# Kernel optimization log

Hardware: AMD Instinct MI355X
Metric: run time of the kernel (lower is better)

Reference implementation:

```python
import jax, jax.numpy as jnp
import numpy as np

D_MODEL = 1024
N_HEADS = 16
D_K = D_MODEL // N_HEADS
D_FF = 4096
EPS = 1e-5


def layer_norm(x, g, b):
    mu = jnp.mean(x, axis=-1, keepdims=True)
    var = jnp.var(x, axis=-1, keepdims=True)
    return (x - mu) * jax.lax.rsqrt(var + EPS) * g + b


def setup_inputs() -> dict:
    key = jax.random.key(0)
    ks = jax.random.split(key, 16)
    B, S = 4, 2048
    s_in = 1.0 / np.sqrt(D_MODEL)
    s_ff = 1.0 / np.sqrt(D_FF)
    return {
        "x": jax.random.normal(ks[0], (B, S, D_MODEL), jnp.float32),
        "mask": jnp.ones((B, 1, 1, S), jnp.int32),
        "Wq": jax.random.normal(ks[1], (D_MODEL, D_MODEL), jnp.float32) * s_in,
        "bq": jnp.zeros((D_MODEL,), jnp.float32),
        "Wk": jax.random.normal(ks[2], (D_MODEL, D_MODEL), jnp.float32) * s_in,
        "bk": jnp.zeros((D_MODEL,), jnp.float32),
        "Wv": jax.random.normal(ks[3], (D_MODEL, D_MODEL), jnp.float32) * s_in,
        "bv": jnp.zeros((D_MODEL,), jnp.float32),
        "Wo": jax.random.normal(ks[4], (D_MODEL, D_MODEL), jnp.float32) * s_in,
        "bo": jnp.zeros((D_MODEL,), jnp.float32),
        "W1": jax.random.normal(ks[5], (D_MODEL, D_FF), jnp.float32) * s_in,
        "b1": jnp.zeros((D_FF,), jnp.float32),
        "W2": jax.random.normal(ks[6], (D_FF, D_MODEL), jnp.float32) * s_ff,
        "b2": jnp.zeros((D_MODEL,), jnp.float32),
        "ln1_g": jnp.ones((D_MODEL,), jnp.float32),
        "ln1_b": jnp.zeros((D_MODEL,), jnp.float32),
        "ln2_g": jnp.ones((D_MODEL,), jnp.float32),
        "ln2_b": jnp.zeros((D_MODEL,), jnp.float32),
    }


def reference(x, mask, Wq, bq, Wk, bk, Wv, bv, Wo, bo, W1, b1, W2, b2,
              ln1_g, ln1_b, ln2_g, ln2_b):
    B, S, _ = x.shape
    h = layer_norm(x, ln1_g, ln1_b)  # norm1(x), used for q/k/v
    # project and split heads: [B,S,D] -> [B,H,S,Dk]
    def heads(t):
        return t.reshape(B, S, N_HEADS, D_K).transpose(0, 2, 1, 3)
    Q = heads(h @ Wq + bq)
    K = heads(h @ Wk + bk)
    V = heads(h @ Wv + bv)
    scores = jnp.einsum('bhqd,bhkd->bhqk', Q, K) / jnp.sqrt(jnp.float32(D_K))
    scores = jnp.where(mask == 0, jnp.float32(-1e9), scores)
    attn = jax.nn.softmax(scores, axis=-1)
    out = jnp.einsum('bhqk,bhkd->bhqd', attn, V)
    out = out.transpose(0, 2, 1, 3).reshape(B, S, D_MODEL)
    attn_out = out @ Wo + bo
    x = x + attn_out
    # FFN with pre-norm (torch nn.GELU default = exact erf gelu)
    h2 = layer_norm(x, ln2_g, ln2_b)
    ff = jax.nn.gelu(h2 @ W1 + b1, approximate=False) @ W2 + b2
    return x + ff
```

## Files before the change

### kernel.cpp

```cpp
#include <hip/hip_runtime.h>
#include <stdint.h>
#include <string.h>


typedef unsigned int       u32;
typedef unsigned short     u16;
typedef __bf16 bf16x8 __attribute__((ext_vector_type(8)));
typedef float  floatx4 __attribute__((ext_vector_type(4)));

#define D_MODEL 1024
#define N_HEADS 16
#define D_K     64
#define D_FF    4096
#define S_LEN   2048
#define N_TOK   8192
#define LDQKV   3072

__device__ __forceinline__ u16 f2b(float f) {
    u32 u = __float_as_uint(f);
    u32 r = (u + 0x7fffu + ((u >> 16) & 1u)) >> 16;
    return (u16)r;
}

__device__ __forceinline__ float fast_gelu(float x) {
    float t = x * x;
    float y = x * 1.5957691216057308f * fmaf(t, 0.044715f, 1.0f);
    return x * __builtin_amdgcn_rcpf(1.0f + __expf(-y));
}

__device__ __forceinline__ void gl_lds16(const void* g, void* l) {
    __builtin_amdgcn_global_load_lds(
        (const __attribute__((address_space(1))) u32*)g,
        (__attribute__((address_space(3))) u32*)l, 16, 0, 0);
}

__global__ __launch_bounds__(256) void transpose_bf16_kernel(
    const float* __restrict__ src, u16* __restrict__ dst, int R, int C)
{
    __shared__ float tile[32][33];
    int cb = blockIdx.x * 32, rb = blockIdx.y * 32;
    int tx = threadIdx.x & 31, ty = threadIdx.x >> 5;
    #pragma unroll
    for (int yy = ty; yy < 32; yy += 8)
        tile[yy][tx] = src[(size_t)(rb + yy) * C + cb + tx];
    __syncthreads();
    #pragma unroll
    for (int yy = ty; yy < 32; yy += 8)
        dst[(size_t)(cb + yy) * R + rb + tx] = f2b(tile[tx][yy]);
}

__global__ __launch_bounds__(256) void vt_kernel(
    const u16* __restrict__ Qkv, u16* __restrict__ Vt)
{
    __shared__ u32 tile[64 * 65];
    int b = blockIdx.z, h = blockIdx.y, s0 = blockIdx.x * 64;
    int t = threadIdx.x;
    int r = t >> 2, cg = (t & 3) * 16;
    const u16* src = &Qkv[((size_t)(b * S_LEN + s0 + r)) * LDQKV + 2048 + h * D_K + cg];
    uint4 a0 = *(const uint4*)src;
    uint4 a1 = *(const uint4*)(src + 8);
    u16 vals[16];
    memcpy(vals, &a0, 16); memcpy(vals + 8, &a1, 16);
    #pragma unroll
    for (int j = 0; j < 16; j++) tile[r * 65 + cg + j] = vals[j];
    __syncthreads();
    int f = t & 63, w = t >> 6;
    u16 outv[16];
    #pragma unroll
    for (int j = 0; j < 16; j++) outv[j] = (u16)tile[(w * 16 + j) * 65 + f];
    uint4 o0, o1; memcpy(&o0, outv, 16); memcpy(&o1, outv + 8, 16);
    u16* dst = &Vt[((size_t)((b * N_HEADS + h) * D_K + f)) * S_LEN + s0 + w * 16];
    *(uint4*)dst = o0; *(uint4*)(dst + 8) = o1;
}

__global__ __launch_bounds__(256) void ln_kernel(
    const float* __restrict__ x, const float* __restrict__ g,
    const float* __restrict__ b, u16* __restrict__ out)
{
    int row = blockIdx.x;
    int t = threadIdx.x;
    const float4* xr = reinterpret_cast<const float4*>(x + (size_t)row * D_MODEL);
    float4 v = xr[t];
    float s  = v.x + v.y + v.z + v.w;
    float ss = v.x * v.x + v.y * v.y + v.z * v.z + v.w * v.w;
    #pragma unroll
    for (int off = 32; off >= 1; off >>= 1) {
        s  += __shfl_down(s,  off);
        ss += __shfl_down(ss, off);
    }
    __shared__ float red[8];
    int wid = t >> 6, ln = t & 63;
    if (ln == 0) { red[wid] = s; red[4 + wid] = ss; }
    __syncthreads();
    float S  = red[0] + red[1] + red[2] + red[3];
    float SS = red[4] + red[5] + red[6] + red[7];
    float mu  = S * (1.0f / D_MODEL);
    float var = SS * (1.0f / D_MODEL) - mu * mu;
    float rs  = rsqrtf(var + 1e-5f);
    const float4* g4 = reinterpret_cast<const float4*>(g);
    const float4* b4 = reinterpret_cast<const float4*>(b);
    float4 gv = g4[t], bv = b4[t];
    float y0 = (v.x - mu) * rs * gv.x + bv.x;
    float y1 = (v.y - mu) * rs * gv.y + bv.y;
    float y2 = (v.z - mu) * rs * gv.z + bv.z;
    float y3 = (v.w - mu) * rs * gv.w + bv.w;
    uint2 pk;
    pk.x = (u32)f2b(y0) | ((u32)f2b(y1) << 16);
    pk.y = (u32)f2b(y2) | ((u32)f2b(y3) << 16);
    *reinterpret_cast<uint2*>(out + (size_t)row * D_MODEL + t * 4) = pk;
}

template<int MT>
__global__ __launch_bounds__(256) void gemm_bt(
    const u16* __restrict__ A, const u16* __restrict__ Bt,
    const float* __restrict__ bias, const float* __restrict__ biasK,
    const float* __restrict__ biasV, const float* __restrict__ resid,
    float* __restrict__ outF, u16* __restrict__ outB,
    int M, int N, int K, int flags)
{
    constexpr int ATILES = MT / 32;
    __shared__ u16 As[MT * 64];
    __shared__ u16 Bs[128 * 64];

    int nbx = N >> 7, nby = M / MT;
    int bid = blockIdx.x;
    int xcd = bid & 7, p = bid >> 3;
    int bandsz = nby >> 3;
    int m0 = (xcd * bandsz + p / nbx) * MT;
    int n0 = (p % nbx) * 128;

    int t = threadIdx.x;
    int wave = t >> 6, lane = t & 63, quad = lane >> 4, lr = lane & 15;
    int wm = (wave >> 1) * (MT / 2), wn = (wave & 1) * 64;

    floatx4 acc[ATILES][4] = {};

    for (int k0 = 0; k0 < K; k0 += 64) {
        #pragma unroll
        for (int i = 0; i < MT / 32; i++) {
            int s = t + i * 256;
            int row = s >> 3, g = ((s & 7) ^ (row & 7)) * 8;
            gl_lds16(&A[(size_t)(m0 + row) * K + k0 + g], &As[s * 8]);
        }
        #pragma unroll
        for (int i = 0; i < 4; i++) {
            int s = t + i * 256;
            int row = s >> 3, g = ((s & 7) ^ (row & 7)) * 8;
            gl_lds16(&Bt[(size_t)(n0 + row) * K + k0 + g], &Bs[s * 8]);
        }
        __syncthreads();

        #pragma unroll
        for (int kk = 0; kk < 2; kk++) {
            bf16x8 af[ATILES], bfr[4];
            #pragma unroll
            for (int mt = 0; mt < ATILES; mt++) {
                int row = wm + mt * 16 + lr;
                int pg = ((kk * 4 + quad) ^ (row & 7)) * 8;
                af[mt] = *reinterpret_cast<const bf16x8*>(&As[row * 64 + pg]);
            }
            #pragma unroll
            for (int nt = 0; nt < 4; nt++) {
                int row = wn + nt * 16 + lr;
                int pg = ((kk * 4 + quad) ^ (row & 7)) * 8;
                bfr[nt] = *reinterpret_cast<const bf16x8*>(&Bs[row * 64 + pg]);
            }
            #pragma unroll
            for (int mt = 0; mt < ATILES; mt++)
                #pragma unroll
                for (int nt = 0; nt < 4; nt++)
                    acc[mt][nt] = __builtin_amdgcn_mfma_f32_16x16x32_bf16(
                        af[mt], bfr[nt], acc[mt][nt], 0, 0, 0);
        }
        __syncthreads();
    }

    bool do_gelu = (flags & 1) != 0;
    #pragma unroll
    for (int mt = 0; mt < ATILES; mt++) {
        #pragma unroll
        for (int nt = 0; nt < 4; nt++) {
            int c = n0 + wn + nt * 16 + lr;
            float bsv;
            if (biasK) {
                if (c >= 2048)      bsv = biasV[c - 2048];
                else if (c >= 1024) bsv = biasK[c - 1024];
                else                bsv = bias[c];
            } else {
                bsv = bias[c];
            }
            #pragma unroll
            for (int i = 0; i < 4; i++) {
                int r = m0 + wm + mt * 16 + quad * 4 + i;
                float v = acc[mt][nt][i] + bsv;
                if (resid) v += resid[(size_t)r * N + c];
                if (do_gelu) v = fast_gelu(v);
                if (outF) outF[(size_t)r * N + c] = v;
                if (outB) outB[(size_t)r * N + c] = f2b(v);
            }
        }
    }
}

__global__ __launch_bounds__(256, 4) void attn_mfma_kernel(
    const u16* __restrict__ Qkv, const u16* __restrict__ Vt,
    const int* __restrict__ mask, u16* __restrict__ ctx)
{
    __shared__ u16 Ks[64 * 72];
    __shared__ u16 Vs[64 * 72];
    __shared__ u16 Ps[128 * 72];
    __shared__ float Ms[64];

    int b = blockIdx.z, h = blockIdx.y;
    int q0 = blockIdx.x * 128;
    int t = threadIdx.x;
    int wave = t >> 6, lane = t & 63, quad = lane >> 4, lr = lane & 15;
    int wm = wave * 32;

    bf16x8 qf[2][2];
    #pragma unroll
    for (int mt = 0; mt < 2; mt++)
        #pragma unroll
        for (int kk = 0; kk < 2; kk++)
            qf[mt][kk] = *(const bf16x8*)&Qkv[((size_t)(b * S_LEN + q0 + wm + mt * 16 + lr)) * LDQKV
                                              + h * D_K + kk * 32 + quad * 8];

    floatx4 o[2][4] = {};
    float lsum[2][4] = {};
    const float kS = 0.125f * 1.4426950408889634f;

    for (int kt = 0; kt < S_LEN / 64; kt++) {
        __syncthreads();
        {
            int row = t >> 2, cg = (t & 3) * 16;
            const u16* kg = &Qkv[((size_t)(b * S_LEN + kt * 64 + row)) * LDQKV + 1024 + h * D_K + cg];
            *(uint4*)&Ks[row * 72 + cg]     = *(const uint4*)kg;
            *(uint4*)&Ks[row * 72 + cg + 8] = *(const uint4*)(kg + 8);
            const u16* vg = &Vt[((size_t)((b * N_HEADS + h) * D_K + row)) * S_LEN + kt * 64 + cg];
            *(uint4*)&Vs[row * 72 + cg]     = *(const uint4*)vg;
            *(uint4*)&Vs[row * 72 + cg + 8] = *(const uint4*)(vg + 8);
            if (t < 64) Ms[t] = (mask[b * S_LEN + kt * 64 + t] == 0) ? -1e30f : 0.0f;
        }
        __syncthreads();

        floatx4 s[2][4] = {};
        {
            bf16x8 bk[2][4];
            #pragma unroll
            for (int kk = 0; kk < 2; kk++)
                #pragma unroll
                for (int n = 0; n < 4; n++)
                    bk[kk][n] = *(const bf16x8*)&Ks[(n * 16 + lr) * 72 + kk * 32 + quad * 8];
            __builtin_amdgcn_s_setprio(1);
            #pragma unroll
            for (int kk = 0; kk < 2; kk++)
                #pragma unroll
                for (int mt = 0; mt < 2; mt++)
                    #pragma unroll
                    for (int n = 0; n < 4; n++)
                        s[mt][n] = __builtin_amdgcn_mfma_f32_16x16x32_bf16(
                            qf[mt][kk], bk[kk][n], s[mt][n], 0, 0, 0);
            __builtin_amdgcn_s_setprio(0);
        }

        #pragma unroll
        for (int mt = 0; mt < 2; mt++) {
            #pragma unroll
            for (int n = 0; n < 4; n++) {
                float msk = Ms[n * 16 + lr];
                float p0 = __builtin_amdgcn_exp2f(fmaf(s[mt][n][0], kS, msk));
                float p1 = __builtin_amdgcn_exp2f(fmaf(s[mt][n][1], kS, msk));
                float p2 = __builtin_amdgcn_exp2f(fmaf(s[mt][n][2], kS, msk));
                float p3 = __builtin_amdgcn_exp2f(fmaf(s[mt][n][3], kS, msk));
                lsum[mt][0] += p0; lsum[mt][1] += p1;
                lsum[mt][2] += p2; lsum[mt][3] += p3;
                u32 pkA, pkB;
                asm("v_cvt_pk_bf16_f32 %0, %1, %2" : "=v"(pkA) : "v"(p0), "v"(p1));
                asm("v_cvt_pk_bf16_f32 %0, %1, %2" : "=v"(pkB) : "v"(p2), "v"(p3));
                int base = (wm + mt * 16 + quad * 4) * 72 + n * 16 + lr;
                Ps[base]           = (u16)(pkA & 0xffffu);
                Ps[base + 72]      = (u16)(pkA >> 16);
                Ps[base + 144]     = (u16)(pkB & 0xffffu);
                Ps[base + 216]     = (u16)(pkB >> 16);
            }
        }

        bf16x8 bv[4][2];
        #pragma unroll
        for (int kk = 0; kk < 2; kk++)
            #pragma unroll
            for (int n = 0; n < 4; n++)
                bv[n][kk] = *(const bf16x8*)&Vs[(n * 16 + lr) * 72 + kk * 32 + quad * 8];

        __syncthreads();

        __builtin_amdgcn_s_setprio(1);
        #pragma unroll
        for (int kk = 0; kk < 2; kk++) {
            #pragma unroll
            for (int mt = 0; mt < 2; mt++) {
                bf16x8 ap = *(const bf16x8*)&Ps[(wm + mt * 16 + lr) * 72 + kk * 32 + quad * 8];
                #pragma unroll
                for (int n = 0; n < 4; n++)
                    o[mt][n] = __builtin_amdgcn_mfma_f32_16x16x32_bf16(
                        ap, bv[n][kk], o[mt][n], 0, 0, 0);
            }
        }
        __builtin_amdgcn_s_setprio(0);
    }

    #pragma unroll
    for (int mt = 0; mt < 2; mt++)
        #pragma unroll
        for (int i = 0; i < 4; i++) {
            float v = lsum[mt][i];
            v += __shfl_xor(v, 1);
            v += __shfl_xor(v, 2);
            v += __shfl_xor(v, 4);
            v += __shfl_xor(v, 8);
            lsum[mt][i] = 1.0f / v;
        }
    #pragma unroll
    for (int mt = 0; mt < 2; mt++)
        #pragma unroll
        for (int n = 0; n < 4; n++)
            #pragma unroll
            for (int i = 0; i < 4; i++) {
                int row = q0 + wm + mt * 16 + quad * 4 + i;
                int col = h * D_K + n * 16 + lr;
                ctx[((size_t)(b * S_LEN + row)) * D_MODEL + col] =
                    f2b(o[mt][n][i] * lsum[mt][i]);
            }
}

extern "C" void kernel_launch(void* const* d_in, const int* in_sizes, int n_in,
                              void* d_out, int out_size, void* d_ws, size_t ws_size,
                              hipStream_t stream)
{
    const float* x    = (const float*)d_in[0];
    const int*   mask = (const int*)  d_in[1];
    const float* Wq   = (const float*)d_in[2];
    const float* bq   = (const float*)d_in[3];
    const float* Wk   = (const float*)d_in[4];
    const float* bk   = (const float*)d_in[5];
    const float* Wv   = (const float*)d_in[6];
    const float* bv   = (const float*)d_in[7];
    const float* Wo   = (const float*)d_in[8];
    const float* bo   = (const float*)d_in[9];
    const float* W1   = (const float*)d_in[10];
    const float* b1   = (const float*)d_in[11];
    const float* W2   = (const float*)d_in[12];
    const float* b2   = (const float*)d_in[13];
    const float* ln1g = (const float*)d_in[14];
    const float* ln1b = (const float*)d_in[15];
    const float* ln2g = (const float*)d_in[16];
    const float* ln2b = (const float*)d_in[17];
    float* out = (float*)d_out;

    char* ws = (char*)d_ws;
    const size_t MB = 1u << 20;
    u16*   wqkvT = (u16*)(ws + 0 * MB);
    u16*   woT   = (u16*)(ws + 6 * MB);
    u16*   w1T   = (u16*)(ws + 8 * MB);
    u16*   w2T   = (u16*)(ws + 16 * MB);
    u16*   h     = (u16*)(ws + 24 * MB);
    u16*   Qkv   = (u16*)(ws + 40 * MB);
    u16*   ctx   = (u16*)(ws + 88 * MB);
    float* x1    = (float*)(ws + 104 * MB);
    u16*   Vt    = h;

    bool full = ws_size >= 216 * MB;
    u16* h2  = full ? (u16*)(ws + 136 * MB) : Qkv;
    u16* ff1 = full ? (u16*)(ws + 152 * MB) : (u16*)(ws + 56 * MB);
    int nchunk = full ? 1 : 2;
    int Mc = N_TOK / nchunk;

    dim3 blk(256);

    transpose_bf16_kernel<<<dim3(32, 32),  blk, 0, stream>>>(Wq, wqkvT,             1024, 1024);
    transpose_bf16_kernel<<<dim3(32, 32),  blk, 0, stream>>>(Wk, wqkvT + 1024*1024, 1024, 1024);
    transpose_bf16_kernel<<<dim3(32, 32),  blk, 0, stream>>>(Wv, wqkvT + 2048*1024, 1024, 1024);
    transpose_bf16_kernel<<<dim3(32, 32),  blk, 0, stream>>>(Wo, woT, 1024, 1024);
    transpose_bf16_kernel<<<dim3(128, 32), blk, 0, stream>>>(W1, w1T, 1024, 4096);
    transpose_bf16_kernel<<<dim3(32, 128), blk, 0, stream>>>(W2, w2T, 4096, 1024);

    ln_kernel<<<N_TOK, blk, 0, stream>>>(x, ln1g, ln1b, h);

    gemm_bt<128><<<dim3(24 * 64), blk, 0, stream>>>(h, wqkvT, bq, bk, bv, nullptr,
                                                    nullptr, Qkv, N_TOK, LDQKV, D_MODEL, 0);

    vt_kernel<<<dim3(32, 16, 4), blk, 0, stream>>>(Qkv, Vt);

    attn_mfma_kernel<<<dim3(16, 16, 4), blk, 0, stream>>>(Qkv, Vt, mask, ctx);

    gemm_bt<64><<<dim3(8 * 128), blk, 0, stream>>>(ctx, woT, bo, nullptr, nullptr, x,
                                                   x1, nullptr, N_TOK, D_MODEL, D_MODEL, 0);

    ln_kernel<<<N_TOK, blk, 0, stream>>>(x1, ln2g, ln2b, h2);

    for (int c = 0; c < nchunk; c++) {
        size_t ro = (size_t)c * Mc * D_MODEL;
        size_t rf = (size_t)c * Mc * D_FF;
        gemm_bt<128><<<dim3(32 * (Mc / 128)), blk, 0, stream>>>(
            h2 + ro, w1T, b1, nullptr, nullptr, nullptr,
            nullptr, ff1 + (full ? rf : 0), Mc, D_FF, D_MODEL, 1);
        gemm_bt<64><<<dim3(8 * (Mc / 64)), blk, 0, stream>>>(
            ff1 + (full ? rf : 0), w2T, b2, nullptr, nullptr, x1 + ro,
            out + ro, nullptr, Mc, D_MODEL, D_FF, 0);
    }
}
```

Before: 606.1 us.

## Fuse V transpose into QKV GEMM epilogue and transpose score MFMA layout

The QKV GEMM epilogue now writes V columns directly in transposed [b,h,d,s] layout, which removes the separate vt_kernel launch and its extra read/write pass over V. The attention kernel swaps the MFMA operand order so each lane holds four consecutive keys for one query. This lets the mask load as a float4, the row sum accumulate per lane, and P be stored to LDS as a packed 8-byte write instead of four scattered u16 stores. The softmax uses __expf with a 0.125 scale instead of exp2 with a folded constant. Vt gets its own workspace region, and the final normalisation reduces across quads and then broadcasts with shuffles.

```diff
diff --git a/kernel.cpp b/kernel.cpp
--- a/kernel.cpp
+++ b/kernel.cpp
@@ -47,30 +47,6 @@
     #pragma unroll
     for (int yy = ty; yy < 32; yy += 8)
         dst[(size_t)(cb + yy) * R + rb + tx] = f2b(tile[tx][yy]);
-}
-
-__global__ __launch_bounds__(256) void vt_kernel(
-    const u16* __restrict__ Qkv, u16* __restrict__ Vt)
-{
-    __shared__ u32 tile[64 * 65];
-    int b = blockIdx.z, h = blockIdx.y, s0 = blockIdx.x * 64;
-    int t = threadIdx.x;
-    int r = t >> 2, cg = (t & 3) * 16;
-    const u16* src = &Qkv[((size_t)(b * S_LEN + s0 + r)) * LDQKV + 2048 + h * D_K + cg];
-    uint4 a0 = *(const uint4*)src;
-    uint4 a1 = *(const uint4*)(src + 8);
-    u16 vals[16];
-    memcpy(vals, &a0, 16); memcpy(vals + 8, &a1, 16);
-    #pragma unroll
-    for (int j = 0; j < 16; j++) tile[r * 65 + cg + j] = vals[j];
-    __syncthreads();
-    int f = t & 63, w = t >> 6;
-    u16 outv[16];
-    #pragma unroll
-    for (int j = 0; j < 16; j++) outv[j] = (u16)tile[(w * 16 + j) * 65 + f];
-    uint4 o0, o1; memcpy(&o0, outv, 16); memcpy(&o1, outv + 8, 16);
-    u16* dst = &Vt[((size_t)((b * N_HEADS + h) * D_K + f)) * S_LEN + s0 + w * 16];
-    *(uint4*)dst = o0; *(uint4*)(dst + 8) = o1;
 }
 
 __global__ __launch_bounds__(256) void ln_kernel(
@@ -115,7 +91,7 @@
     const u16* __restrict__ A, const u16* __restrict__ Bt,
     const float* __restrict__ bias, const float* __restrict__ biasK,
     const float* __restrict__ biasV, const float* __restrict__ resid,
-    float* __restrict__ outF, u16* __restrict__ outB,
+    float* __restrict__ outF, u16* __restrict__ outB, u16* __restrict__ outVt,
     int M, int N, int K, int flags)
 {
     constexpr int ATILES = MT / 32;
@@ -189,6 +165,17 @@
             } else {
                 bsv = bias[c];
             }
+            if (outVt && c >= 2048) {
+                int r0 = m0 + wm + mt * 16 + quad * 4;
+                int hb = (c - 2048) >> 6, f = (c - 2048) & 63;
+                int bb = r0 >> 11, sIn = r0 & 2047;
+                u32 w0 = (u32)f2b(acc[mt][nt][0] + bsv) | ((u32)f2b(acc[mt][nt][1] + bsv) << 16);
+                u32 w1 = (u32)f2b(acc[mt][nt][2] + bsv) | ((u32)f2b(acc[mt][nt][3] + bsv) << 16);
+                uint2 pk2; pk2.x = w0; pk2.y = w1;
+                *reinterpret_cast<uint2*>(
+                    &outVt[((size_t)((bb * N_HEADS + hb) * D_K + f)) * S_LEN + sIn]) = pk2;
+                continue;
+            }
             #pragma unroll
             for (int i = 0; i < 4; i++) {
                 int r = m0 + wm + mt * 16 + quad * 4 + i;
@@ -226,8 +213,7 @@
                                               + h * D_K + kk * 32 + quad * 8];
 
     floatx4 o[2][4] = {};
-    float lsum[2][4] = {};
-    const float kS = 0.125f * 1.4426950408889634f;
+    float lsum[2] = {0.0f, 0.0f};
 
     for (int kt = 0; kt < S_LEN / 64; kt++) {
         __syncthreads();
@@ -259,7 +245,7 @@
                     #pragma unroll
                     for (int n = 0; n < 4; n++)
                         s[mt][n] = __builtin_amdgcn_mfma_f32_16x16x32_bf16(
-                            qf[mt][kk], bk[kk][n], s[mt][n], 0, 0, 0);
+                            bk[kk][n], qf[mt][kk], s[mt][n], 0, 0, 0);
             __builtin_amdgcn_s_setprio(0);
         }
 
@@ -267,21 +253,17 @@
         for (int mt = 0; mt < 2; mt++) {
             #pragma unroll
             for (int n = 0; n < 4; n++) {
-                float msk = Ms[n * 16 + lr];
-                float p0 = __builtin_amdgcn_exp2f(fmaf(s[mt][n][0], kS, msk));
-                float p1 = __builtin_amdgcn_exp2f(fmaf(s[mt][n][1], kS, msk));
-                float p2 = __builtin_amdgcn_exp2f(fmaf(s[mt][n][2], kS, msk));
-                float p3 = __builtin_amdgcn_exp2f(fmaf(s[mt][n][3], kS, msk));
-                lsum[mt][0] += p0; lsum[mt][1] += p1;
-                lsum[mt][2] += p2; lsum[mt][3] += p3;
-                u32 pkA, pkB;
-                asm("v_cvt_pk_bf16_f32 %0, %1, %2" : "=v"(pkA) : "v"(p0), "v"(p1));
-                asm("v_cvt_pk_bf16_f32 %0, %1, %2" : "=v"(pkB) : "v"(p2), "v"(p3));
-                int base = (wm + mt * 16 + quad * 4) * 72 + n * 16 + lr;
-                Ps[base]           = (u16)(pkA & 0xffffu);
-                Ps[base + 72]      = (u16)(pkA >> 16);
-                Ps[base + 144]     = (u16)(pkB & 0xffffu);
-                Ps[base + 216]     = (u16)(pkB >> 16);
+                const float4 mv = *reinterpret_cast<const float4*>(&Ms[n * 16 + quad * 4]);
+                float p0 = __expf(fmaf(s[mt][n][0], 0.125f, mv.x));
+                float p1 = __expf(fmaf(s[mt][n][1], 0.125f, mv.y));
+                float p2 = __expf(fmaf(s[mt][n][2], 0.125f, mv.z));
+                float p3 = __expf(fmaf(s[mt][n][3], 0.125f, mv.w));
+                lsum[mt] += (p0 + p1) + (p2 + p3);
+                u32 w0, w1;
+                asm("v_cvt_pk_bf16_f32 %0, %1, %2" : "=v"(w0) : "v"(p0), "v"(p1));
+                asm("v_cvt_pk_bf16_f32 %0, %1, %2" : "=v"(w1) : "v"(p2), "v"(p3));
+                uint2 pk2; pk2.x = w0; pk2.y = w1;
+                *reinterpret_cast<uint2*>(&Ps[(wm + mt * 16 + lr) * 72 + n * 16 + quad * 4]) = pk2;
             }
         }
 
@@ -309,19 +291,19 @@
         __builtin_amdgcn_s_setprio(0);
     }
 
-    #pragma unroll
-    for (int mt = 0; mt < 2; mt++)
-        #pragma unroll
-        for (int i = 0; i < 4; i++) {
-            float v = lsum[mt][i];
-            v += __shfl_xor(v, 1);
-            v += __shfl_xor(v, 2);
-            v += __shfl_xor(v, 4);
-            v += __shfl_xor(v, 8);
-            lsum[mt][i] = 1.0f / v;
-        }
-    #pragma unroll
-    for (int mt = 0; mt < 2; mt++)
+    float inv[2];
+    #pragma unroll
+    for (int mt = 0; mt < 2; mt++) {
+        float v = lsum[mt];
+        v += __shfl_xor(v, 16);
+        v += __shfl_xor(v, 32);
+        inv[mt] = 1.0f / v;
+    }
+    #pragma unroll
+    for (int mt = 0; mt < 2; mt++) {
+        float iv[4];
+        #pragma unroll
+        for (int i = 0; i < 4; i++) iv[i] = __shfl(inv[mt], quad * 4 + i);
         #pragma unroll
         for (int n = 0; n < 4; n++)
             #pragma unroll
@@ -329,8 +311,9 @@
                 int row = q0 + wm + mt * 16 + quad * 4 + i;
                 int col = h * D_K + n * 16 + lr;
                 ctx[((size_t)(b * S_LEN + row)) * D_MODEL + col] =
-                    f2b(o[mt][n][i] * lsum[mt][i]);
-            }
+                    f2b(o[mt][n][i] * iv[i]);
+            }
+    }
 }
 
 extern "C" void kernel_launch(void* const* d_in, const int* in_sizes, int n_in,
@@ -367,9 +350,9 @@
     u16*   Qkv   = (u16*)(ws + 40 * MB);
     u16*   ctx   = (u16*)(ws + 88 * MB);
     float* x1    = (float*)(ws + 104 * MB);
-    u16*   Vt    = h;
 
     bool full = ws_size >= 216 * MB;
+    u16* Vt = full ? (u16*)(ws + 184 * MB) : (u16*)(ws + 104 * MB);
     u16* h2  = full ? (u16*)(ws + 136 * MB) : Qkv;
     u16* ff1 = full ? (u16*)(ws + 152 * MB) : (u16*)(ws + 56 * MB);
     int nchunk = full ? 1 : 2;
@@ -387,14 +370,12 @@
     ln_kernel<<<N_TOK, blk, 0, stream>>>(x, ln1g, ln1b, h);
 
     gemm_bt<128><<<dim3(24 * 64), blk, 0, stream>>>(h, wqkvT, bq, bk, bv, nullptr,
-                                                    nullptr, Qkv, N_TOK, LDQKV, D_MODEL, 0);
-
-    vt_kernel<<<dim3(32, 16, 4), blk, 0, stream>>>(Qkv, Vt);
+                                                    nullptr, Qkv, Vt, N_TOK, LDQKV, D_MODEL, 0);
 
     attn_mfma_kernel<<<dim3(16, 16, 4), blk, 0, stream>>>(Qkv, Vt, mask, ctx);
 
     gemm_bt<64><<<dim3(8 * 128), blk, 0, stream>>>(ctx, woT, bo, nullptr, nullptr, x,
-                                                   x1, nullptr, N_TOK, D_MODEL, D_MODEL, 0);
+                                                   x1, nullptr, nullptr, N_TOK, D_MODEL, D_MODEL, 0);
 
     ln_kernel<<<N_TOK, blk, 0, stream>>>(x1, ln2g, ln2b, h2);
 
@@ -403,9 +384,9 @@
         size_t rf = (size_t)c * Mc * D_FF;
         gemm_bt<128><<<dim3(32 * (Mc / 128)), blk, 0, stream>>>(
             h2 + ro, w1T, b1, nullptr, nullptr, nullptr,
-            nullptr, ff1 + (full ? rf : 0), Mc, D_FF, D_MODEL, 1);
+            nullptr, ff1 + (full ? rf : 0), nullptr, Mc, D_FF, D_MODEL, 1);
         gemm_bt<64><<<dim3(8 * (Mc / 64)), blk, 0, stream>>>(
             ff1 + (full ? rf : 0), w2T, b2, nullptr, nullptr, x1 + ro,
-            out + ro, nullptr, Mc, D_MODEL, D_FF, 0);
-    }
-}
+            out + ro, nullptr, nullptr, Mc, D_MODEL, D_FF, 0);
+    }
+}
```

After: 580.1 us. 1.04x faster.
